# Kernel tuning notes

Measured on AMD Instinct MI355X. Metric: run time of the kernel, lower is better.

## Reference

```python
import jax, jax.numpy as jnp
import numpy as np

B, T, N_ITEMS, DIM, L = 512, 50, 10000, 128, 4
H = DIM // 2


def setup_inputs() -> dict:
    key = jax.random.key(0)
    ks = jax.random.split(key, 16)
    emb = jax.random.normal(ks[0], (N_ITEMS + 1, DIM), jnp.float32) * 0.02
    emb = emb.at[0].set(0.0)  # padding_idx=0
    s = 1.0 / np.sqrt(DIM)
    inp = {
        "users": jax.random.randint(ks[1], (B,), 0, B),
        "user_seq": jax.random.randint(ks[2], (B, T), 0, N_ITEMS + 1),
        "pos_items": jax.random.randint(ks[3], (B,), 0, N_ITEMS),
        "neg_items": jax.random.randint(ks[4], (B, 10), 0, N_ITEMS),
        "pos_labels": jnp.ones((B,), jnp.float32),
        "neg_labels": jnp.zeros((B, 10), jnp.float32),
        "base_model_preds": jax.random.normal(ks[5], (B, N_ITEMS), jnp.float32),
        "emb": emb,
        "lstm_wih": jax.random.uniform(ks[6], (4 * DIM, DIM), jnp.float32, -s, s),
        "lstm_whh": jax.random.uniform(ks[7], (4 * DIM, DIM), jnp.float32, -s, s),
        "lstm_bih": jax.random.uniform(ks[8], (4 * DIM,), jnp.float32, -s, s),
        "lstm_bhh": jax.random.uniform(ks[9], (4 * DIM,), jnp.float32, -s, s),
        "wl_W1": jax.random.normal(ks[10], (L, 2 * DIM, H), jnp.float32) * 0.05,
        "wl_b1": jax.random.normal(ks[11], (L, H), jnp.float32) * 0.01,
        "wl_W2": jax.random.normal(ks[12], (L, H), jnp.float32) * 0.05,
        "wl_b2": jax.random.normal(ks[13], (L,), jnp.float32) * 0.01,
        "alphas": jnp.ones((L,), jnp.float32) / L,
    }
    return inp


def _lstm_last(x, wih, whh, bih, bhh):
    # x: [B, T, D]; torch gate order i, f, g, o. Returns last hidden state [B, D].
    Bx, _, D = x.shape
    bias = bih + bhh

    def step(carry, xt):
        h, c = carry
        gates = xt @ wih.T + h @ whh.T + bias  # [B, 4D]
        i, f, g, o = jnp.split(gates, 4, axis=-1)
        c = jax.nn.sigmoid(f) * c + jax.nn.sigmoid(i) * jnp.tanh(g)
        h = jax.nn.sigmoid(o) * jnp.tanh(c)
        return (h, c), None

    init = (jnp.zeros((Bx, D), x.dtype), jnp.zeros((Bx, D), x.dtype))
    (h, _), _ = jax.lax.scan(step, init, x.transpose(1, 0, 2))
    return h


def reference(users, user_seq, pos_items, neg_items, pos_labels, neg_labels,
              base_model_preds, emb, lstm_wih, lstm_whh, lstm_bih, lstm_bhh,
              wl_W1, wl_b1, wl_W2, wl_b2, alphas):
    seq_emb = emb[user_seq]                      # [B, T, D]
    seq_repr = _lstm_last(seq_emb, lstm_wih, lstm_whh, lstm_bih, lstm_bhh)  # [B, D]
    item_emb = emb[jnp.arange(N_ITEMS)]          # [N, D]

    # Weak learners: Linear(2D->H) split algebraically into seq/item matmuls
    # to avoid materializing the [B, N, 2D] broadcast-concat tensor.
    final_scores = jnp.zeros((seq_repr.shape[0], N_ITEMS), seq_repr.dtype)
    for l in range(L):
        sp = seq_repr @ wl_W1[l, :DIM]           # [B, H]
        ip = item_emb @ wl_W1[l, DIM:]           # [N, H]
        hid = jax.nn.relu(sp[:, None, :] + ip[None, :, :] + wl_b1[l])  # [B, N, H]
        scores = hid @ wl_W2[l] + wl_b2[l]       # [B, N]
        final_scores = final_scores + alphas[l] * scores

    pos_scores = jnp.take_along_axis(final_scores, pos_items[:, None], axis=1)  # [B, 1]
    neg_scores = jnp.take_along_axis(final_scores, neg_items, axis=1)           # [B, n_neg]
    loss = jnp.mean(jnp.exp(-(pos_scores - neg_scores)))
    return final_scores, loss
```

## Files before the change

### kernel.cpp

```cpp
#include <hip/hip_runtime.h>
#include <stdint.h>

typedef uint32_t u32;
typedef uint16_t u16;
typedef uint64_t u64;
typedef __attribute__((ext_vector_type(4))) float f32x4;
typedef __attribute__((ext_vector_type(8))) short bf16x8;
typedef __attribute__((ext_vector_type(2))) _Float16 f16x2;

#define NI   10000
#define NPAD 10240
#define L2E  1.4426950408889634f

#define DEV static __device__ __forceinline__

DEV float asf(u32 u){ union{u32 i; float f;} v; v.i=u; return v.f; }
DEV u32   asu(float f){ union{u32 i; float f;} v; v.f=f; return v.i; }
DEV float bf2f(u16 u){ return asf(((u32)u)<<16); }
DEV u16   f2bf(float f){ u32 i = asu(f); return (u16)((i + 0x7fffu + ((i>>16)&1u))>>16); }
DEV u16   f2h(float f){ _Float16 h = (_Float16)f; return __builtin_bit_cast(u16, h); }
DEV f32x4 fzero(){ f32x4 z; z[0]=0.f; z[1]=0.f; z[2]=0.f; z[3]=0.f; return z; }

DEV void gl2lds16(const void* g, void* l){
  __builtin_amdgcn_global_load_lds((const __attribute__((address_space(1))) u32*)g,
                                   (__attribute__((address_space(3))) u32*)l, 16, 0, 0);
}

__global__ void k_prep(const int* __restrict__ seq, const float* __restrict__ emb,
                       const float* __restrict__ wih, const float* __restrict__ bih,
                       const float* __restrict__ bhh, const float* __restrict__ W1,
                       const float* __restrict__ b1, const float* __restrict__ W2,
                       const float* __restrict__ alphas,
                       u16* __restrict__ EMB16, u16* __restrict__ XG, u16* __restrict__ Wih16,
                       u16* __restrict__ W1s16, u16* __restrict__ W1i16,
                       float* __restrict__ bias512, float* __restrict__ b1k,
                       float* __restrict__ w2h, u32* __restrict__ w2p)
{
  const int tid = blockIdx.x*blockDim.x + threadIdx.x;
  const int nth = gridDim.x*blockDim.x;
  for (int e = tid; e < 10001*128; e += nth) EMB16[e] = f2bf(emb[e]);
  for (int e = tid; e < 25600*128; e += nth){ int r = e>>7, d = e&127;
      int t = r>>9, b = r&511;
      XG[e] = f2bf(emb[(size_t)seq[b*50 + t]*128 + d]); }
  for (int e = tid; e < 512*128; e += nth){ int col = e>>7;
      float sc = ((col>>7)==2) ? 2.0f*L2E : L2E;
      Wih16[e] = f2bf(wih[e]*sc); }
  for (int e = tid; e < 256*128; e += nth){ int k = e>>7, d = e&127; int l = k>>6, h = k&63;
      W1s16[e] = f2bf(W1[l*16384 + d*64 + h]); }
  for (int e = tid; e < 256*128; e += nth){ int k = e>>7, d = e&127; int l = k>>6, h = k&63;
      W1i16[e] = f2bf(W1[l*16384 + (128+d)*64 + h]); }
  for (int e = tid; e < 512; e += nth){
      float sc = ((e>>7)==2) ? 2.0f*L2E : L2E;
      bias512[e] = (bih[e] + bhh[e])*sc; }
  for (int e = tid; e < 256; e += nth){ int l = e>>6, h = e&63;
      b1k[e] = b1[l*64 + h]; w2h[e] = 0.5f*alphas[l]*W2[l*64 + h]; }
  for (int e = tid; e < 128; e += nth){
      int k0 = 2*e, k1 = 2*e+1;
      float w0 = 0.5f*alphas[k0>>6]*W2[(k0>>6)*64 + (k0&63)];
      float w1 = 0.5f*alphas[k1>>6]*W2[(k1>>6)*64 + (k1&63)];
      w2p[e] = (u32)f2h(w0) | ((u32)f2h(w1)<<16); }
}

template<int OUT_MODE, int BIAS_MODE>
DEV void gemm_body(const u16* __restrict__ A, const u16* __restrict__ BT,
                   const float* __restrict__ bias, void* __restrict__ Cout,
                   int Nvalid, int ldc, int bx, int by, char* smem)
{
  u16* sA = (u16*)smem;
  u16* sB = (u16*)(smem + 32768);
  const int tid = threadIdx.x, l = tid&63, w = tid>>6;
  const int c16 = l&15, g4 = l>>4;
  const int m0 = bx*128, n0 = by*64;
  #pragma unroll
  for (int it=0; it<4; ++it){
    int row = it*32 + w*4 + g4;
    int sg  = c16 ^ (row&7);
    gl2lds16(A + (size_t)(m0+row)*128 + sg*8, (char*)sA + (it*32 + w*4)*256);
  }
  #pragma unroll
  for (int it=0; it<2; ++it){
    int row = it*32 + w*4 + g4;
    int srow;
    if constexpr (OUT_MODE==4){
      int base1 = (by>>2)*256 + (by&3)*32;
      srow = base1 + (row&31) + (row>>5)*128;
    } else {
      srow = n0 + row; if (srow >= Nvalid) srow = Nvalid-1;
    }
    int sg  = c16 ^ (row&7);
    gl2lds16(BT + (size_t)srow*128 + sg*8, (char*)sB + (it*32 + w*4)*256);
  }
  __syncthreads();
  f32x4 acc[4];
  #pragma unroll
  for (int ct=0; ct<4; ++ct) acc[ct] = fzero();
  #pragma unroll
  for (int kt=0; kt<4; ++kt){
    bf16x8 a, b[4];
    int arow = w*16 + c16;
    a = *(const bf16x8*)((const char*)sA + arow*256 + (((kt*4+g4) ^ (arow&7))*16));
    #pragma unroll
    for (int ct=0; ct<4; ++ct){
      int brow = (OUT_MODE==4) ? ((ct>>1)*32 + (ct&1)*16 + c16) : (ct*16 + c16);
      b[ct] = *(const bf16x8*)((const char*)sB + brow*256 + (((kt*4+g4) ^ (brow&7))*16));
    }
    #pragma unroll
    for (int ct=0; ct<4; ++ct)
      acc[ct] = __builtin_amdgcn_mfma_f32_16x16x32_bf16(a, b[ct], acc[ct], 0, 0, 0);
  }
  const int rbase = m0 + w*16 + g4*4;
  if constexpr (OUT_MODE==4){
    int t    = rbase >> 9;
    int bloc = rbase & 511;
    int bb   = bloc >> 4;
    int g4l  = (bloc >> 2) & 3;
    int half = by >> 2;
    #pragma unroll
    for (int p=0; p<2; ++p){
      int colA = (by&3)*32 + p*16 + c16 + (by>>2)*256;
      int colB = colA + 128;
      u32 ws[4];
      #pragma unroll
      for (int i=0;i<4;++i){
        float va = acc[p][i], vb = acc[p+2][i];
        if constexpr (BIAS_MODE==1){ va += bias[colA]; vb += bias[colB]; }
        ws[i] = (u32)f2bf(va) | ((u32)f2bf(vb)<<16);
      }
      int tidl = ((by&3)*2 + p)*64 + g4l*16 + c16;
      char* dst = (char*)Cout + ((size_t)((t*32+bb)*1024 + half*512 + tidl))*16;
      *(f32x4*)dst = *(f32x4*)ws;
    }
  } else {
    #pragma unroll
    for (int ct=0; ct<4; ++ct){
      int col = n0 + ct*16 + c16;
      if (col < Nvalid){
        float v[4];
        #pragma unroll
        for (int i=0;i<4;++i){
          v[i] = acc[ct][i];
          if constexpr (BIAS_MODE==1) v[i] += bias[col];
          else if constexpr (BIAS_MODE==2) v[i] += bias[rbase+i];
        }
        if constexpr (OUT_MODE==0){
          float* C = (float*)Cout;
          #pragma unroll
          for (int i=0;i<4;++i) C[(size_t)(rbase+i)*ldc + col] = v[i];
        } else {
          u32* C = (u32*)Cout;
          u32 w0 = (u32)f2h(v[0]) | ((u32)f2h(v[1])<<16);
          u32 w1 = (u32)f2h(v[2]) | ((u32)f2h(v[3])<<16);
          int kp0 = rbase>>1;
          size_t i32 = ((size_t)(kp0>>2)*ldc + col)*4 + (kp0&3);
          u64 pk = (u64)w0 | ((u64)w1<<32);
          *(u64*)&C[i32] = pk;
        }
      }
    }
  }
}

template<int OUT_MODE, int BIAS_MODE>
__global__ __launch_bounds__(512) void k_gemm(const u16* __restrict__ A,
    const u16* __restrict__ BT, const float* __restrict__ bias,
    void* __restrict__ Cout, int Nvalid, int ldc)
{
  __shared__ __align__(16) char smem[49152];
  gemm_body<OUT_MODE,BIAS_MODE>(A, BT, bias, Cout, Nvalid, ldc, blockIdx.x, blockIdx.y, smem);
}

DEV void lstm_body(const float* __restrict__ whh, const u16* __restrict__ XWL,
                   u16* __restrict__ H16, int bb, char* smem)
{
  const int tid = threadIdx.x, l = tid&63, w = tid>>6;
  const int c16 = l&15, g4 = l>>4;
  const int u = w*16 + c16;
  bf16x8 bfr[4][4];
  #pragma unroll
  for (int j=0; j<4; ++j){
    int col = (j*8 + w)*16 + c16;
    float sc = (j==2) ? 2.0f*L2E : L2E;
    const float* src = whh + (size_t)col*128;
    #pragma unroll
    for (int kt=0; kt<4; ++kt){
      int k0 = kt*32 + g4*8;
      float4 x0 = *(const float4*)(src + k0);
      float4 x1 = *(const float4*)(src + k0 + 4);
      bf16x8 f;
      f[0]=(short)f2bf(x0.x*sc); f[1]=(short)f2bf(x0.y*sc); f[2]=(short)f2bf(x0.z*sc); f[3]=(short)f2bf(x0.w*sc);
      f[4]=(short)f2bf(x1.x*sc); f[5]=(short)f2bf(x1.y*sc); f[6]=(short)f2bf(x1.z*sc); f[7]=(short)f2bf(x1.w*sc);
      bfr[kt][j] = f;
    }
  }
  for (int e = tid; e < 4096; e += 512) ((u16*)smem)[e] = 0;
  int hoff[4];
  #pragma unroll
  for (int i=0;i<4;++i){ int s = g4*4 + i;
    hoff[i] = s*256 + (((u>>3) ^ (s&7))*16) + (u&7)*2; }
  const char* gb = (const char*)XWL;
  {
    size_t base = (size_t)bb*1024;
    gl2lds16(gb + (base + tid)*16,        smem + 8192 + w*1024);
    gl2lds16(gb + (base + 512 + tid)*16,  smem + 8192 + 8192 + w*1024);
  }
  float cst[4] = {0.f,0.f,0.f,0.f};
  float hreg[4] = {0.f,0.f,0.f,0.f};
  __syncthreads();
  #pragma unroll 2
  for (int t=0; t<50; ++t){
    const int cur = t&1;
    char* AhC = smem + cur*4096;
    char* AhN = smem + (cur^1)*4096;
    char* XsC = smem + 8192 + cur*16384;
    char* XsN = smem + 8192 + (cur^1)*16384;
    if (t < 49){
      size_t base = (size_t)((t+1)*32+bb)*1024;
      gl2lds16(gb + (base + tid)*16,       XsN + w*1024);
      gl2lds16(gb + (base + 512 + tid)*16, XsN + 8192 + w*1024);
    }
    bf16x8 xv0 = *(const bf16x8*)(XsC + tid*16);
    bf16x8 xv1 = *(const bf16x8*)(XsC + 8192 + tid*16);
    const u32* W0 = (const u32*)&xv0;
    const u32* W1 = (const u32*)&xv1;
    f32x4 acc[4];
    #pragma unroll
    for (int i=0;i<4;++i){
      acc[0][i] = asf(W0[i]<<16);
      acc[1][i] = asf(W0[i]&0xffff0000u);
      acc[2][i] = asf(W1[i]<<16);
      acc[3][i] = asf(W1[i]&0xffff0000u);
    }
    #pragma unroll
    for (int kt=0; kt<4; ++kt){
      bf16x8 a = *(const bf16x8*)(AhC + c16*256 + (((kt*4+g4) ^ (c16&7))*16));
      #pragma unroll
      for (int j=0; j<4; ++j)
        acc[j] = __builtin_amdgcn_mfma_f32_16x16x32_bf16(a, bfr[kt][j], acc[j], 0, 0, 0);
    }
    #pragma unroll
    for (int i=0;i<4;++i){
      float yi = acc[0][i], yf = acc[1][i], yg = acc[2][i], yo = acc[3][i];
      yg = fminf(fmaxf(yg, -40.f), 40.f);
      float Ei = __builtin_amdgcn_exp2f(-yi);
      float Ef = __builtin_amdgcn_exp2f(-yf);
      float G  = __builtin_amdgcn_exp2f(yg);
      float Eo = __builtin_amdgcn_exp2f(-yo);
      float ai = 1.f+Ei, af = 1.f+Ef, gp = G+1.f, gm = G-1.f;
      float num = fmaf(af, gm, cst[i]*ai*gp);
      float den = af*ai*gp;
      float cn  = num * __builtin_amdgcn_rcpf(den);
      cst[i] = cn;
      float yc = fminf(fmaxf(cn*(2.0f*L2E), -40.f), 40.f);
      float C2 = __builtin_amdgcn_exp2f(yc);
      float h  = (C2-1.f) * __builtin_amdgcn_rcpf((1.f+Eo)*(C2+1.f));
      hreg[i] = h;
      *(u16*)(AhN + hoff[i]) = f2bf(h);
    }
    __syncthreads();
  }
  #pragma unroll
  for (int i=0;i<4;++i)
    H16[(size_t)(bb*16 + g4*4 + i)*128 + u] = f2bf(hreg[i]);
}

__global__ __launch_bounds__(512) void k_lstm_ipf(const float* __restrict__ whh,
    const u16* __restrict__ XWL, u16* __restrict__ H16,
    const u16* __restrict__ W1i16, const u16* __restrict__ EMB16,
    const float* __restrict__ b1k, u32* __restrict__ IPF)
{
  __shared__ __align__(16) char smem[49152];
  if (blockIdx.x < 32){
    lstm_body(whh, XWL, H16, blockIdx.x, smem);
  } else {
    int g = blockIdx.x - 32;
    gemm_body<2,2>(W1i16, EMB16, b1k, IPF, NI, NPAD, g&1, g>>1, smem);
  }
}

__global__ void k_small(const float* __restrict__ SPm, u32* __restrict__ SPH,
                        const float* __restrict__ w2h, float* __restrict__ cB,
                        const u32* __restrict__ IPF, const float* __restrict__ b2,
                        const float* __restrict__ alphas, float* __restrict__ cN)
{
  const int bid = blockIdx.x;
  if (bid < 256){
    int idx = bid*256 + threadIdx.x;
    int b = idx>>7, kp = idx&127;
    float x0 = SPm[(size_t)b*256 + 2*kp], x1 = SPm[(size_t)b*256 + 2*kp + 1];
    SPH[idx] = (u32)f2h(x0) | ((u32)f2h(x1)<<16);
  } else if (bid < 258){
    int b = (bid-256)*256 + threadIdx.x;
    if (b < 512){
      float s = 0.f;
      for (int k=0;k<256;++k) s = fmaf(SPm[(size_t)b*256+k], w2h[k], s);
      cB[b] = s;
    }
  } else {
    int n = (bid-258)*256 + threadIdx.x;
    if (n >= NPAD) return;
    if (n >= NI){ cN[n] = 0.f; return; }
    float cb2 = 0.f;
    #pragma unroll
    for (int l=0;l<4;++l) cb2 += alphas[l]*b2[l];
    float s = cb2;
    for (int kp=0; kp<128; ++kp){
      u32 v = IPF[((size_t)(kp>>2)*NPAD + n)*4 + (kp&3)];
      f16x2 h = __builtin_bit_cast(f16x2, v);
      s = fmaf((float)h.x, w2h[2*kp],   s);
      s = fmaf((float)h.y, w2h[2*kp+1], s);
    }
    cN[n] = s;
  }
}

DEV float fdot2(u32 ab, u32 w, float acc){
  asm("v_dot2_f32_f16 %0, %1, %2, %0" : "+v"(acc) : "v"(ab), "s"(w));
  return acc;
}
typedef __attribute__((ext_vector_type(4))) u32 u32x4;

__global__ __launch_bounds__(256) void k_score(const u32* __restrict__ SPH,
    const u32* __restrict__ IPF, const u32* __restrict__ w2p,
    const float* __restrict__ cB, const float* __restrict__ cN,
    float* __restrict__ out)
{
  const int n  = blockIdx.x*256 + threadIdx.x;
  const int b0 = blockIdx.y*16;
  const float cNv = cN[n];
  float acc[16];
  #pragma unroll
  for (int i=0;i<16;++i) acc[i] = cB[b0+i] + cNv;
  #pragma unroll 1
  for (int c=0;c<4;++c){
    u32x4 iw4[8];
    #pragma unroll
    for (int vv=0; vv<8; ++vv)
      iw4[vv] = ((const u32x4*)IPF)[(size_t)(c*8+vv)*NPAD + n];
    const u32* wp = w2p + c*32;
    #pragma unroll
    for (int i=0;i<16;++i){
      const u32* sp = SPH + (size_t)(b0+i)*128 + c*32;
      float a = acc[i];
      #pragma unroll
      for (int vv=0; vv<8; ++vv){
        #pragma unroll
        for (int q=0; q<4; ++q){
          f16x2 t = __builtin_bit_cast(f16x2, sp[vv*4+q]) + __builtin_bit_cast(f16x2, iw4[vv][q]);
          u32 ta = __builtin_bit_cast(u32, t) & 0x7fff7fffu;
          a = fdot2(ta, wp[vv*4+q], a);
        }
      }
      acc[i] = a;
    }
  }
  if (n < NI){
    #pragma unroll
    for (int i=0;i<16;++i) out[(size_t)(b0+i)*NI + n] = acc[i];
  }
}

__global__ void k_loss(const float* __restrict__ scores, const int* __restrict__ pos,
                       const int* __restrict__ neg, float* __restrict__ outloss)
{
  __shared__ float red[256];
  int tid = threadIdx.x;
  float s = 0.f;
  for (int e = tid; e < 5120; e += 256){
    int b = e/10, j = e - b*10;
    float ps = scores[(size_t)b*NI + pos[b]];
    float ns = scores[(size_t)b*NI + neg[b*10 + j]];
    s += __expf(ns - ps);
  }
  red[tid] = s; __syncthreads();
  for (int st=128; st>0; st>>=1){ if (tid<st) red[tid]+=red[tid+st]; __syncthreads(); }
  if (tid==0) outloss[0] = red[0] * (1.0f/5120.0f);
}

extern "C" void kernel_launch(void* const* d_in, const int* in_sizes, int n_in,
                              void* d_out, int out_size, void* d_ws, size_t ws_size,
                              hipStream_t stream)
{
  const int*   seq    = (const int*)d_in[1];
  const int*   pos    = (const int*)d_in[2];
  const int*   neg    = (const int*)d_in[3];
  const float* emb    = (const float*)d_in[7];
  const float* wih    = (const float*)d_in[8];
  const float* whh    = (const float*)d_in[9];
  const float* bih    = (const float*)d_in[10];
  const float* bhh    = (const float*)d_in[11];
  const float* W1     = (const float*)d_in[12];
  const float* b1     = (const float*)d_in[13];
  const float* W2     = (const float*)d_in[14];
  const float* b2     = (const float*)d_in[15];
  const float* alphas = (const float*)d_in[16];
  float* out = (float*)d_out;
  (void)in_sizes; (void)n_in; (void)out_size; (void)ws_size;

  char* p = (char*)d_ws;
  size_t off = 0;
  auto alloc = [&](size_t bytes)->char*{ char* r = p + off;
      off = (off + bytes + 255) & ~(size_t)255; return r; };
  u16*  EMB16   = (u16*)  alloc((size_t)10001*128*2);
  u16*  XG      = (u16*)  alloc((size_t)25600*128*2);
  u16*  Wih16   = (u16*)  alloc((size_t)512*128*2);
  u16*  W1s16   = (u16*)  alloc((size_t)256*128*2);
  u16*  W1i16   = (u16*)  alloc((size_t)256*128*2);
  float* bias512= (float*)alloc(512*4);
  float* b1k    = (float*)alloc(256*4);
  float* w2h    = (float*)alloc(256*4);
  u32*  w2p     = (u32*)  alloc(128*4);
  u16*  XWL     = (u16*)  alloc((size_t)25600*512*2);
  u16*  H16     = (u16*)  alloc((size_t)512*128*2);
  float* SPm    = (float*)alloc((size_t)512*256*4);
  u32*  SPH     = (u32*)  alloc((size_t)512*128*4);
  u32*  IPF     = (u32*)  alloc((size_t)128*NPAD*4);
  float* cB     = (float*)alloc(512*4);
  float* cN     = (float*)alloc((size_t)NPAD*4);

  k_prep<<<256,256,0,stream>>>(seq, emb, wih, bih, bhh, W1, b1, W2, alphas,
                               EMB16, XG, Wih16, W1s16, W1i16, bias512, b1k, w2h, w2p);
  k_gemm<4,1><<<dim3(200,8),512,0,stream>>>(XG, Wih16, bias512, XWL, 512, 512);
  k_lstm_ipf<<<32 + 314,512,0,stream>>>(whh, XWL, H16, W1i16, EMB16, b1k, IPF);
  k_gemm<0,0><<<dim3(4,4),512,0,stream>>>(H16, W1s16, nullptr, SPm, 256, 256);
  k_small<<<298,256,0,stream>>>(SPm, SPH, w2h, cB, IPF, b2, alphas, cN);
  k_score<<<dim3(40,32),256,0,stream>>>(SPH, IPF, w2p, cB, cN, out);
  k_loss<<<1,256,0,stream>>>(out, pos, neg, out + (size_t)512*NI);
}
```

Before: 198.6 us.

## Fuse embedding gather into input GEMM, merge post kernels, retile score kernel

Removes the materialised XG gather buffer by having the input-projection GEMM gather embedding rows through the sequence indices directly, and vectorises the bf16 conversions in prep. Merges the seq-projection GEMM and the small reduction kernel into one k_post launch that writes fp16 output directly. The per-batch constant is now computed from H16 and a precomputed vector folding W1 and W2 instead of from SPm. IPF changes from an interleaved u32x4 layout to a plain per-kp layout, and k_score drops to 8 batch rows per thread with twice the grid, trading reuse for more parallelism and fewer registers.

```diff
diff --git a/kernel.cpp b/kernel.cpp
--- a/kernel.cpp
+++ b/kernel.cpp
@@ -31,20 +31,32 @@
                        const float* __restrict__ bhh, const float* __restrict__ W1,
                        const float* __restrict__ b1, const float* __restrict__ W2,
                        const float* __restrict__ alphas,
-                       u16* __restrict__ EMB16, u16* __restrict__ XG, u16* __restrict__ Wih16,
+                       u16* __restrict__ EMB16, u16* __restrict__ Wih16,
                        u16* __restrict__ W1s16, u16* __restrict__ W1i16,
                        float* __restrict__ bias512, float* __restrict__ b1k,
-                       float* __restrict__ w2h, u32* __restrict__ w2p)
+                       float* __restrict__ w2h, u32* __restrict__ w2p,
+                       float* __restrict__ qv)
 {
   const int tid = blockIdx.x*blockDim.x + threadIdx.x;
   const int nth = gridDim.x*blockDim.x;
-  for (int e = tid; e < 10001*128; e += nth) EMB16[e] = f2bf(emb[e]);
-  for (int e = tid; e < 25600*128; e += nth){ int r = e>>7, d = e&127;
-      int t = r>>9, b = r&511;
-      XG[e] = f2bf(emb[(size_t)seq[b*50 + t]*128 + d]); }
-  for (int e = tid; e < 512*128; e += nth){ int col = e>>7;
-      float sc = ((col>>7)==2) ? 2.0f*L2E : L2E;
-      Wih16[e] = f2bf(wih[e]*sc); }
+  for (int e = tid; e < 10001*16; e += nth){
+    const float* s = emb + (size_t)e*8;
+    float4 x0 = *(const float4*)s, x1 = *(const float4*)(s+4);
+    bf16x8 o;
+    o[0]=(short)f2bf(x0.x); o[1]=(short)f2bf(x0.y); o[2]=(short)f2bf(x0.z); o[3]=(short)f2bf(x0.w);
+    o[4]=(short)f2bf(x1.x); o[5]=(short)f2bf(x1.y); o[6]=(short)f2bf(x1.z); o[7]=(short)f2bf(x1.w);
+    *(bf16x8*)&EMB16[(size_t)e*8] = o;
+  }
+  for (int e = tid; e < 512*16; e += nth){
+    int col = (e*8)>>7;
+    float sc = ((col>>7)==2) ? 2.0f*L2E : L2E;
+    const float* s = wih + (size_t)e*8;
+    float4 x0 = *(const float4*)s, x1 = *(const float4*)(s+4);
+    bf16x8 o;
+    o[0]=(short)f2bf(x0.x*sc); o[1]=(short)f2bf(x0.y*sc); o[2]=(short)f2bf(x0.z*sc); o[3]=(short)f2bf(x0.w*sc);
+    o[4]=(short)f2bf(x1.x*sc); o[5]=(short)f2bf(x1.y*sc); o[6]=(short)f2bf(x1.z*sc); o[7]=(short)f2bf(x1.w*sc);
+    *(bf16x8*)&Wih16[(size_t)e*8] = o;
+  }
   for (int e = tid; e < 256*128; e += nth){ int k = e>>7, d = e&127; int l = k>>6, h = k&63;
       W1s16[e] = f2bf(W1[l*16384 + d*64 + h]); }
   for (int e = tid; e < 256*128; e += nth){ int k = e>>7, d = e&127; int l = k>>6, h = k&63;
@@ -59,12 +71,21 @@
       float w0 = 0.5f*alphas[k0>>6]*W2[(k0>>6)*64 + (k0&63)];
       float w1 = 0.5f*alphas[k1>>6]*W2[(k1>>6)*64 + (k1&63)];
       w2p[e] = (u32)f2h(w0) | ((u32)f2h(w1)<<16); }
+  for (int d = tid; d < 128; d += nth){
+    float s = 0.f;
+    for (int k=0;k<256;++k){
+      float wv = 0.5f*alphas[k>>6]*W2[(k>>6)*64 + (k&63)];
+      s = fmaf(wv, W1[(k>>6)*16384 + d*64 + (k&63)], s);
+    }
+    qv[d] = s;
+  }
 }
 
 template<int OUT_MODE, int BIAS_MODE>
 DEV void gemm_body(const u16* __restrict__ A, const u16* __restrict__ BT,
                    const float* __restrict__ bias, void* __restrict__ Cout,
-                   int Nvalid, int ldc, int bx, int by, char* smem)
+                   int Nvalid, int ldc, int bx, int by, char* smem,
+                   const int* __restrict__ seq)
 {
   u16* sA = (u16*)smem;
   u16* sB = (u16*)(smem + 32768);
@@ -75,7 +96,13 @@
   for (int it=0; it<4; ++it){
     int row = it*32 + w*4 + g4;
     int sg  = c16 ^ (row&7);
-    gl2lds16(A + (size_t)(m0+row)*128 + sg*8, (char*)sA + (it*32 + w*4)*256);
+    if constexpr (OUT_MODE==4){
+      int b = (m0&511) + row, t = m0>>9;
+      int idx = seq[b*50 + t];
+      gl2lds16(A + (size_t)idx*128 + sg*8, (char*)sA + (it*32 + w*4)*256);
+    } else {
+      gl2lds16(A + (size_t)(m0+row)*128 + sg*8, (char*)sA + (it*32 + w*4)*256);
+    }
   }
   #pragma unroll
   for (int it=0; it<2; ++it){
@@ -146,14 +173,17 @@
           float* C = (float*)Cout;
           #pragma unroll
           for (int i=0;i<4;++i) C[(size_t)(rbase+i)*ldc + col] = v[i];
+        } else if constexpr (OUT_MODE==1){
+          u16* C = (u16*)Cout;
+          #pragma unroll
+          for (int i=0;i<4;++i) C[(size_t)(rbase+i)*ldc + col] = f2h(v[i]);
         } else {
           u32* C = (u32*)Cout;
           u32 w0 = (u32)f2h(v[0]) | ((u32)f2h(v[1])<<16);
           u32 w1 = (u32)f2h(v[2]) | ((u32)f2h(v[3])<<16);
           int kp0 = rbase>>1;
-          size_t i32 = ((size_t)(kp0>>2)*ldc + col)*4 + (kp0&3);
-          u64 pk = (u64)w0 | ((u64)w1<<32);
-          *(u64*)&C[i32] = pk;
+          C[(size_t)kp0*ldc + col]     = w0;
+          C[(size_t)(kp0+1)*ldc + col] = w1;
         }
       }
     }
@@ -163,10 +193,10 @@
 template<int OUT_MODE, int BIAS_MODE>
 __global__ __launch_bounds__(512) void k_gemm(const u16* __restrict__ A,
     const u16* __restrict__ BT, const float* __restrict__ bias,
-    void* __restrict__ Cout, int Nvalid, int ldc)
+    void* __restrict__ Cout, int Nvalid, int ldc, const int* __restrict__ seq)
 {
   __shared__ __align__(16) char smem[49152];
-  gemm_body<OUT_MODE,BIAS_MODE>(A, BT, bias, Cout, Nvalid, ldc, blockIdx.x, blockIdx.y, smem);
+  gemm_body<OUT_MODE,BIAS_MODE>(A, BT, bias, Cout, Nvalid, ldc, blockIdx.x, blockIdx.y, smem, seq);
 }
 
 DEV void lstm_body(const float* __restrict__ whh, const u16* __restrict__ XWL,
@@ -273,30 +303,33 @@
     lstm_body(whh, XWL, H16, blockIdx.x, smem);
   } else {
     int g = blockIdx.x - 32;
-    gemm_body<2,2>(W1i16, EMB16, b1k, IPF, NI, NPAD, g&1, g>>1, smem);
-  }
-}
-
-__global__ void k_small(const float* __restrict__ SPm, u32* __restrict__ SPH,
-                        const float* __restrict__ w2h, float* __restrict__ cB,
-                        const u32* __restrict__ IPF, const float* __restrict__ b2,
-                        const float* __restrict__ alphas, float* __restrict__ cN)
-{
+    gemm_body<2,2>(W1i16, EMB16, b1k, IPF, NI, NPAD, g&1, g>>1, smem, nullptr);
+  }
+}
+
+__global__ __launch_bounds__(512) void k_post(const u16* __restrict__ H16,
+    const u16* __restrict__ W1s16, u16* __restrict__ SPH,
+    const float* __restrict__ qv, float* __restrict__ cB,
+    const u32* __restrict__ IPF, const float* __restrict__ b2,
+    const float* __restrict__ alphas, const float* __restrict__ w2h,
+    float* __restrict__ cN)
+{
+  __shared__ __align__(16) char smem[49152];
   const int bid = blockIdx.x;
-  if (bid < 256){
-    int idx = bid*256 + threadIdx.x;
-    int b = idx>>7, kp = idx&127;
-    float x0 = SPm[(size_t)b*256 + 2*kp], x1 = SPm[(size_t)b*256 + 2*kp + 1];
-    SPH[idx] = (u32)f2h(x0) | ((u32)f2h(x1)<<16);
-  } else if (bid < 258){
-    int b = (bid-256)*256 + threadIdx.x;
-    if (b < 512){
-      float s = 0.f;
-      for (int k=0;k<256;++k) s = fmaf(SPm[(size_t)b*256+k], w2h[k], s);
-      cB[b] = s;
-    }
+  if (bid < 16){
+    gemm_body<1,0>(H16, W1s16, nullptr, SPH, 256, 256, bid&3, bid>>2, smem, nullptr);
+  } else if (bid == 16){
+    int b = threadIdx.x;
+    float s = 0.f;
+    #pragma unroll
+    for (int d8=0; d8<16; ++d8){
+      bf16x8 hv = *(const bf16x8*)&H16[(size_t)b*128 + d8*8];
+      #pragma unroll
+      for (int j=0;j<8;++j) s = fmaf(bf2f((u16)hv[j]), qv[d8*8+j], s);
+    }
+    cB[b] = s;
   } else {
-    int n = (bid-258)*256 + threadIdx.x;
+    int n = (bid-17)*512 + threadIdx.x;
     if (n >= NPAD) return;
     if (n >= NI){ cN[n] = 0.f; return; }
     float cb2 = 0.f;
@@ -304,8 +337,7 @@
     for (int l=0;l<4;++l) cb2 += alphas[l]*b2[l];
     float s = cb2;
     for (int kp=0; kp<128; ++kp){
-      u32 v = IPF[((size_t)(kp>>2)*NPAD + n)*4 + (kp&3)];
-      f16x2 h = __builtin_bit_cast(f16x2, v);
+      f16x2 h = __builtin_bit_cast(f16x2, IPF[(size_t)kp*NPAD + n]);
       s = fmaf((float)h.x, w2h[2*kp],   s);
       s = fmaf((float)h.y, w2h[2*kp+1], s);
     }
@@ -317,7 +349,6 @@
   asm("v_dot2_f32_f16 %0, %1, %2, %0" : "+v"(acc) : "v"(ab), "s"(w));
   return acc;
 }
-typedef __attribute__((ext_vector_type(4))) u32 u32x4;
 
 __global__ __launch_bounds__(256) void k_score(const u32* __restrict__ SPH,
     const u32* __restrict__ IPF, const u32* __restrict__ w2p,
@@ -325,37 +356,33 @@
     float* __restrict__ out)
 {
   const int n  = blockIdx.x*256 + threadIdx.x;
-  const int b0 = blockIdx.y*16;
+  const int b0 = blockIdx.y*8;
   const float cNv = cN[n];
-  float acc[16];
-  #pragma unroll
-  for (int i=0;i<16;++i) acc[i] = cB[b0+i] + cNv;
+  float acc[8];
+  #pragma unroll
+  for (int i=0;i<8;++i) acc[i] = cB[b0+i] + cNv;
   #pragma unroll 1
   for (int c=0;c<4;++c){
-    u32x4 iw4[8];
-    #pragma unroll
-    for (int vv=0; vv<8; ++vv)
-      iw4[vv] = ((const u32x4*)IPF)[(size_t)(c*8+vv)*NPAD + n];
+    u32 iw[32];
+    #pragma unroll
+    for (int v=0; v<32; ++v) iw[v] = IPF[(size_t)(c*32+v)*NPAD + n];
     const u32* wp = w2p + c*32;
     #pragma unroll
-    for (int i=0;i<16;++i){
+    for (int i=0;i<8;++i){
       const u32* sp = SPH + (size_t)(b0+i)*128 + c*32;
       float a = acc[i];
       #pragma unroll
-      for (int vv=0; vv<8; ++vv){
-        #pragma unroll
-        for (int q=0; q<4; ++q){
-          f16x2 t = __builtin_bit_cast(f16x2, sp[vv*4+q]) + __builtin_bit_cast(f16x2, iw4[vv][q]);
-          u32 ta = __builtin_bit_cast(u32, t) & 0x7fff7fffu;
-          a = fdot2(ta, wp[vv*4+q], a);
-        }
+      for (int v=0; v<32; ++v){
+        f16x2 t = __builtin_bit_cast(f16x2, sp[v]) + __builtin_bit_cast(f16x2, iw[v]);
+        u32 ta = __builtin_bit_cast(u32, t) & 0x7fff7fffu;
+        a = fdot2(ta, wp[v], a);
       }
       acc[i] = a;
     }
   }
   if (n < NI){
     #pragma unroll
-    for (int i=0;i<16;++i) out[(size_t)(b0+i)*NI + n] = acc[i];
+    for (int i=0;i<8;++i) out[(size_t)(b0+i)*NI + n] = acc[i];
   }
 }
 
@@ -401,7 +428,6 @@
   auto alloc = [&](size_t bytes)->char*{ char* r = p + off;
       off = (off + bytes + 255) & ~(size_t)255; return r; };
   u16*  EMB16   = (u16*)  alloc((size_t)10001*128*2);
-  u16*  XG      = (u16*)  alloc((size_t)25600*128*2);
   u16*  Wih16   = (u16*)  alloc((size_t)512*128*2);
   u16*  W1s16   = (u16*)  alloc((size_t)256*128*2);
   u16*  W1i16   = (u16*)  alloc((size_t)256*128*2);
@@ -409,20 +435,19 @@
   float* b1k    = (float*)alloc(256*4);
   float* w2h    = (float*)alloc(256*4);
   u32*  w2p     = (u32*)  alloc(128*4);
+  float* qv     = (float*)alloc(128*4);
   u16*  XWL     = (u16*)  alloc((size_t)25600*512*2);
   u16*  H16     = (u16*)  alloc((size_t)512*128*2);
-  float* SPm    = (float*)alloc((size_t)512*256*4);
-  u32*  SPH     = (u32*)  alloc((size_t)512*128*4);
+  u16*  SPH     = (u16*)  alloc((size_t)512*256*2);
   u32*  IPF     = (u32*)  alloc((size_t)128*NPAD*4);
   float* cB     = (float*)alloc(512*4);
   float* cN     = (float*)alloc((size_t)NPAD*4);
 
-  k_prep<<<256,256,0,stream>>>(seq, emb, wih, bih, bhh, W1, b1, W2, alphas,
-                               EMB16, XG, Wih16, W1s16, W1i16, bias512, b1k, w2h, w2p);
-  k_gemm<4,1><<<dim3(200,8),512,0,stream>>>(XG, Wih16, bias512, XWL, 512, 512);
+  k_prep<<<512,256,0,stream>>>(seq, emb, wih, bih, bhh, W1, b1, W2, alphas,
+                               EMB16, Wih16, W1s16, W1i16, bias512, b1k, w2h, w2p, qv);
+  k_gemm<4,1><<<dim3(200,8),512,0,stream>>>(EMB16, Wih16, bias512, XWL, 512, 512, seq);
   k_lstm_ipf<<<32 + 314,512,0,stream>>>(whh, XWL, H16, W1i16, EMB16, b1k, IPF);
-  k_gemm<0,0><<<dim3(4,4),512,0,stream>>>(H16, W1s16, nullptr, SPm, 256, 256);
-  k_small<<<298,256,0,stream>>>(SPm, SPH, w2h, cB, IPF, b2, alphas, cN);
-  k_score<<<dim3(40,32),256,0,stream>>>(SPH, IPF, w2p, cB, cN, out);
+  k_post<<<37,512,0,stream>>>(H16, W1s16, SPH, qv, cB, IPF, b2, alphas, w2h, cN);
+  k_score<<<dim3(40,64),256,0,stream>>>((const u32*)SPH, IPF, w2p, cB, cN, out);
   k_loss<<<1,256,0,stream>>>(out, pos, neg, out + (size_t)512*NI);
 }
```

After: 184.0 us. 7.3% less time.
